# Performance work log

Measured on AMD Instinct MI355X. Metric: run time of the kernel, lower is better.

## Reference

```python
import jax, jax.numpy as jnp
import numpy as np

B, T, D = 2, 2048, 1024
H = 16
HD = D // H  # head_dim = 64 (kv_rank == embed_dim)
INT4_MIN, INT4_MAX = -8.0, 7.0


def _int4_quant_dequant(x):
    # per-token amax over last dim (head_dim), as in INT4Quantizer with 4-D input
    amax = jnp.max(jnp.abs(x), axis=-1, keepdims=True)
    amax = jnp.maximum(amax, 1e-5)
    scale = amax / 7.0
    q = jnp.clip(jnp.round(x / scale), INT4_MIN, INT4_MAX)  # stored as int8 in cache
    return q * scale


def setup_inputs() -> dict:
    key = jax.random.key(0)
    ks = jax.random.split(key, 11)
    s = 1.0 / np.sqrt(D)
    return {
        "query": jax.random.normal(ks[0], (B, T, D), jnp.float32),
        "key": jax.random.normal(ks[1], (B, T, D), jnp.float32),
        "value": jax.random.normal(ks[2], (B, T, D), jnp.float32),
        "Wq": jax.random.normal(ks[3], (D, D), jnp.float32) * s,
        "bq": jnp.zeros((D,), jnp.float32),
        "Wk": jax.random.normal(ks[4], (D, D), jnp.float32) * s,
        "bk": jnp.zeros((D,), jnp.float32),
        "Wv": jax.random.normal(ks[5], (D, D), jnp.float32) * s,
        "bv": jnp.zeros((D,), jnp.float32),
        "Wo": jax.random.normal(ks[6], (D, D), jnp.float32) * s,
        "bo": jnp.zeros((D,), jnp.float32),
    }


def reference(query, key, value, Wq, bq, Wk, bk, Wv, bv, Wo, bo):
    # projections (nn.Linear: x @ W.T + b)
    q = query @ Wq.T + bq
    k = key @ Wk.T + bk
    v = value @ Wv.T + bv
    # (B, T, D) -> (B, H, T, HD)
    q = q.reshape(B, T, H, HD).transpose(0, 2, 1, 3)
    k = k.reshape(B, T, H, HD).transpose(0, 2, 1, 3)
    v = v.reshape(B, T, H, HD).transpose(0, 2, 1, 3)
    # INT4 quantized KV cache update (use_cache=True): quantize -> scatter into
    # fresh cache -> dequantize the just-written block == quant/dequant of k, v
    k = _int4_quant_dequant(k)
    v = _int4_quant_dequant(v)
    # attention
    scale = HD ** (-0.5)
    attn = jnp.einsum("bhqd,bhkd->bhqk", q, k) * scale
    attn = jax.nn.softmax(attn.astype(jnp.float32), axis=-1).astype(query.dtype)
    out = jnp.einsum("bhqk,bhkd->bhqd", attn, v)
    out = out.transpose(0, 2, 1, 3).reshape(B, T, D)
    out = out @ Wo.T + bo
    return out
```

## Files before the change

### kernel.cpp

```cpp
#include <hip/hip_runtime.h>

typedef unsigned short u16;
typedef unsigned int u32;
typedef float f32x4 __attribute__((ext_vector_type(4)));
typedef float f32x16 __attribute__((ext_vector_type(16)));
typedef short s16x8 __attribute__((ext_vector_type(8)));
typedef u16 u16x8 __attribute__((ext_vector_type(8)));
typedef u16 u16x4 __attribute__((ext_vector_type(4)));
typedef u32 u32x4 __attribute__((ext_vector_type(4)));
typedef _Float16 h16x8 __attribute__((ext_vector_type(8)));
typedef _Float16 h16x2 __attribute__((ext_vector_type(2)));

#define B_ 2
#define T_ 2048
#define H_ 16
#define D_ 1024
#define HD_ 64
#define NTOK (B_*T_)

#define QSCALE 0.18033688011112042f

__device__ __forceinline__ u16 f2b(float f){
  u32 u = __float_as_uint(f);
  return (u16)((u + 0x7fffu + ((u>>16)&1u)) >> 16);
}
__device__ __forceinline__ float b2f(u16 h){ return __uint_as_float(((u32)h)<<16); }

__device__ __forceinline__ void gload_lds16(const u16* g, u16* s){
  __builtin_amdgcn_global_load_lds((const __attribute__((address_space(1))) void*)g,
                                   (__attribute__((address_space(3))) void*)s, 16, 0, 0);
}

template<int ROWS, int WAVES>
__device__ __forceinline__ void stage_tile(const u16* __restrict__ g, size_t ldg,
                                           u16* s, int tid){
  const int w = tid>>6, l = tid&63;
  const int rw = ROWS/WAVES;
  #pragma unroll
  for (int i=0;i<ROWS/(WAVES*8);i++){
    int r0 = w*rw + i*8;
    int r  = r0 + (l>>3);
    int u  = (l&7) ^ (r&7);
    gload_lds16(g + (size_t)r*ldg + (size_t)u*8, s + r0*64);
  }
}

__device__ __forceinline__ u16x8 read_frag(const u16* s, int r, int kk, int l){
  int u = (kk<<2) | (l>>4);
  int phys = u ^ (r&7);
  return *(const u16x8*)(s + r*64 + phys*8);
}
__device__ __forceinline__ u16x8 rfragT(const u16* s, int r, int ks, int hi){
  int phys = (ks*2 + hi) ^ (r&7);
  return *(const u16x8*)(s + r*64 + phys*8);
}

__device__ __forceinline__ void stage_tile32(const u16* __restrict__ g, size_t ldg,
                                             u16* s, int tid){
  const int w = tid>>6, l = tid&63;
  int r0 = w*16;
  int r  = r0 + (l>>2);
  int v  = (l&3) ^ ((r>>1)&3);
  gload_lds16(g + (size_t)r*ldg + (size_t)v*8, s + r0*32);
}
__device__ __forceinline__ u16x8 read_frag32(const u16* s, int r, int l){
  int phys = (l>>4) ^ ((r>>1)&3);
  return *(const u16x8*)(s + r*32 + phys*8);
}

__device__ __forceinline__ f32x4 mfma16_f16(u16x8 a, u16x8 b, f32x4 c){
  return __builtin_amdgcn_mfma_f32_16x16x32_f16(
      __builtin_bit_cast(h16x8,a), __builtin_bit_cast(h16x8,b), c, 0,0,0);
}
__device__ __forceinline__ f32x4 mfma16_bf16(u16x8 a, u16x8 b, f32x4 c){
  return __builtin_amdgcn_mfma_f32_16x16x32_bf16(
      __builtin_bit_cast(s16x8,a), __builtin_bit_cast(s16x8,b), c, 0,0,0);
}
__device__ __forceinline__ f32x16 mfma32_f16(u16x8 a, u16x8 b, f32x16 c){
  return __builtin_amdgcn_mfma_f32_32x32x16_f16(
      __builtin_bit_cast(h16x8,a), __builtin_bit_cast(h16x8,b), c, 0,0,0);
}

__device__ __forceinline__ float ex2(float x){
#if __has_builtin(__builtin_amdgcn_exp2f)
  return __builtin_amdgcn_exp2f(x);
#else
  return exp2f(x);
#endif
}
__device__ __forceinline__ u32 pk2(float a, float b){
  u16 x = __builtin_bit_cast(u16, (_Float16)a);
  u16 y = __builtin_bit_cast(u16, (_Float16)b);
  return (u32)x | ((u32)y<<16);
}
__device__ __forceinline__ float dot2acc(u32 wv, float c){
#if __has_builtin(__builtin_amdgcn_fdot2)
  h16x2 one2 = {(_Float16)1.0f, (_Float16)1.0f};
  return __builtin_amdgcn_fdot2(__builtin_bit_cast(h16x2, wv), one2, c, false);
#else
  h16x2 v = __builtin_bit_cast(h16x2, wv);
  return c + (float)v[0] + (float)v[1];
#endif
}

__device__ __forceinline__ void split_bf4(const float* in, u16* hi, u16* lo, int i){
  f32x4 v = ((const f32x4*)in)[i];
  u16x4 h, lw;
  #pragma unroll
  for (int j=0;j<4;j++){
    u16 hb = f2b(v[j]);
    h[j] = hb;
    lw[j] = f2b(v[j] - b2f(hb));
  }
  ((u16x4*)hi)[i] = h;
  ((u16x4*)lo)[i] = lw;
}
__device__ __forceinline__ void split_h4(const float* in, u16* out, int i){
  f32x4 v = ((const f32x4*)in)[i];
  u16x4 o;
  #pragma unroll
  for (int j=0;j<4;j++){
    _Float16 t = (_Float16)v[j];
    o[j] = __builtin_bit_cast(u16, t);
  }
  ((u16x4*)out)[i] = o;
}

__global__ void split_inputs_kernel(const float* __restrict__ q, const float* __restrict__ k,
                                    const float* __restrict__ v,
                                    u16* __restrict__ qh, u16* __restrict__ khi, u16* __restrict__ klo,
                                    u16* __restrict__ vhi, u16* __restrict__ vlo){
  int i = blockIdx.x*256 + threadIdx.x;
  int which = blockIdx.y;
  if (which==0)      split_h4 (q, qh, i);
  else if (which==1) split_bf4(k, khi, klo, i);
  else               split_bf4(v, vhi, vlo, i);
}

__global__ void split_weights_kernel(const float* __restrict__ wq, const float* __restrict__ wk,
                                     const float* __restrict__ wv, const float* __restrict__ wo,
                                     u16* __restrict__ wqh, u16* __restrict__ wkh, u16* __restrict__ wkl,
                                     u16* __restrict__ wvh, u16* __restrict__ wvl, u16* __restrict__ woh){
  int i = blockIdx.x*256 + threadIdx.x;
  int which = blockIdx.y;
  if (which==0)      split_h4 (wq, wqh, i);
  else if (which==1) split_bf4(wk, wkh, wkl, i);
  else if (which==2) split_bf4(wv, wvh, wvl, i);
  else               split_h4 (wo, woh, i);
}

template<int F16OUT>
__global__ __launch_bounds__(512)
void gemm1(const u16* __restrict__ Ah, const u16* __restrict__ Wh,
           const float* __restrict__ bias, void* __restrict__ Cout, float oscale)
{
  __shared__ u16 sA[2][128*64];
  __shared__ u16 sW[2][64*64];
  const int tid = threadIdx.x, l = tid&63, l15 = l&15, g = l>>4, w = tid>>6;
  const int wm = w>>1, wn = w&1;
  const int bm = blockIdx.x, bn = blockIdx.y;
  const u16* A0 = Ah + (size_t)bm*128*D_;
  const u16* W0 = Wh + (size_t)bn*64*D_;
  f32x4 acc[2][2] = {};

  stage_tile<128,8>(A0, D_, sA[0], tid);
  stage_tile<64 ,8>(W0, D_, sW[0], tid);
  __syncthreads();
  for (int t=0; t<D_/64; ++t){
    const int cur = t&1;
    if (t+1 < D_/64){
      stage_tile<128,8>(A0 + (t+1)*64, D_, sA[cur^1], tid);
      stage_tile<64 ,8>(W0 + (t+1)*64, D_, sW[cur^1], tid);
    }
    #pragma unroll
    for (int kk=0;kk<2;kk++){
      u16x8 af[2], wf[2];
      #pragma unroll
      for (int fm=0;fm<2;fm++) af[fm] = read_frag(sA[cur], wm*32+fm*16+l15, kk, l);
      #pragma unroll
      for (int fn=0;fn<2;fn++) wf[fn] = read_frag(sW[cur], wn*32+fn*16+l15, kk, l);
      #pragma unroll
      for (int fm=0;fm<2;fm++)
        #pragma unroll
        for (int fn=0;fn<2;fn++)
          acc[fm][fn] = mfma16_f16(af[fm], wf[fn], acc[fm][fn]);
    }
    __syncthreads();
  }

  #pragma unroll
  for (int fn=0; fn<2; fn++){
    int col = bn*64 + wn*32 + fn*16 + l15;
    float bv = bias[col];
    #pragma unroll
    for (int fm=0; fm<2; fm++){
      int r0 = bm*128 + wm*32 + fm*16 + g*4;
      #pragma unroll
      for (int j=0;j<4;j++){
        float v = (acc[fm][fn][j] + bv) * oscale;
        if constexpr (F16OUT){
          ((_Float16*)Cout)[(size_t)(r0+j)*D_ + col] = (_Float16)v;
        } else {
          ((float*)Cout)[(size_t)(r0+j)*D_ + col] = v;
        }
      }
    }
  }
}

template<int QMODE>
__global__ __launch_bounds__(512)
void gemm3_quant(const u16* __restrict__ Ah, const u16* __restrict__ Al,
                 const u16* __restrict__ Wh, const u16* __restrict__ Wl,
                 const float* __restrict__ bias, u16* __restrict__ Out)
{
  extern __shared__ u16 sm[];
  const int tid = threadIdx.x, l = tid&63, w = tid>>6, l15 = l&15, g = l>>4;
  const int wm = w>>1, wn = w&1;
  const int bm = blockIdx.x, bn = blockIdx.y;
  const u16* A0 = Ah + (size_t)bm*128*D_;
  const u16* A1 = Al + (size_t)bm*128*D_;
  const u16* W0 = Wh + (size_t)bn*128*D_;
  const u16* W1 = Wl + (size_t)bn*128*D_;
  constexpr int TS = 128*32;
  f32x4 acc[2][4] = {};

  auto stage = [&](int buf, int t){
    u16* base = sm + buf*4*TS;
    stage_tile32(A0 + t*32, D_, base       , tid);
    stage_tile32(A1 + t*32, D_, base +   TS, tid);
    stage_tile32(W0 + t*32, D_, base + 2*TS, tid);
    stage_tile32(W1 + t*32, D_, base + 3*TS, tid);
  };
  stage(0,0);
  __syncthreads();
  for (int t=0; t<D_/32; ++t){
    const int cur = t&1;
    if (t+1 < D_/32) stage(cur^1, t+1);
    const u16* base = sm + cur*4*TS;
    u16x8 ahh[2], ahl[2], whh[4], whl[4];
    #pragma unroll
    for (int fm=0;fm<2;fm++){
      ahh[fm] = read_frag32(base     , wm*32+fm*16+l15, l);
      ahl[fm] = read_frag32(base+  TS, wm*32+fm*16+l15, l);
    }
    #pragma unroll
    for (int fn=0;fn<4;fn++){
      whh[fn] = read_frag32(base+2*TS, wn*64+fn*16+l15, l);
      whl[fn] = read_frag32(base+3*TS, wn*64+fn*16+l15, l);
    }
    #pragma unroll
    for (int fm=0;fm<2;fm++)
      #pragma unroll
      for (int fn=0;fn<4;fn++){
        acc[fm][fn] = mfma16_bf16(ahh[fm], whh[fn], acc[fm][fn]);
        acc[fm][fn] = mfma16_bf16(ahh[fm], whl[fn], acc[fm][fn]);
        acc[fm][fn] = mfma16_bf16(ahl[fm], whh[fn], acc[fm][fn]);
      }
    __syncthreads();
  }

  #pragma unroll
  for (int fn=0;fn<4;fn++){
    float bv = bias[bn*128 + wn*64 + fn*16 + l15];
    #pragma unroll
    for (int fm=0;fm<2;fm++)
      #pragma unroll
      for (int j=0;j<4;j++) acc[fm][fn][j] += bv;
  }

  u16 (*sdq)[136] = (u16(*)[136])sm;
  #pragma unroll
  for (int fm=0;fm<2;fm++)
    #pragma unroll
    for (int j=0;j<4;j++){
      float a = 0.f;
      #pragma unroll
      for (int fn=0;fn<4;fn++) a = fmaxf(a, fabsf(acc[fm][fn][j]));
      a = fmaxf(a, __shfl_xor(a,1)); a = fmaxf(a, __shfl_xor(a,2));
      a = fmaxf(a, __shfl_xor(a,4)); a = fmaxf(a, __shfl_xor(a,8));
      a = fmaxf(a, 1e-5f);
      float scale = a / 7.0f;
      int row = wm*32 + fm*16 + g*4 + j;
      #pragma unroll
      for (int fn=0;fn<4;fn++){
        float q = rintf(acc[fm][fn][j] / scale);
        q = fminf(fmaxf(q, -8.f), 7.f);
        _Float16 dq = (_Float16)(q * scale);
        int col = wn*64 + fn*16 + l15;
        if (QMODE==1) sdq[row][col] = __builtin_bit_cast(u16, dq);
        else          sdq[col][row] = __builtin_bit_cast(u16, dq);
      }
    }
  __syncthreads();

  if (QMODE==1){
    int r = tid>>2, seg = tid&3;
    u16* dst = Out + (size_t)(bm*128 + r)*D_ + bn*128 + seg*32;
    #pragma unroll
    for (int i=0;i<4;i++)
      *(u16x8*)(dst + i*8) = *(const u16x8*)&sdq[r][seg*32 + i*8];
  } else {
    int cc = tid>>2, seg = tid&3;
    int hh = 2*bn + (cc>>6), dd = cc&63, b = bm>>4;
    u16* dst = Out + ((size_t)((b*H_+hh)*HD_ + dd))*T_ + (bm&15)*128 + seg*32;
    #pragma unroll
    for (int i=0;i<4;i++)
      *(u16x8*)(dst + i*8) = *(const u16x8*)&sdq[cc][seg*32 + i*8];
  }
}

__global__ __launch_bounds__(256)
void attn_kernel(const _Float16* __restrict__ Qp, const u16* __restrict__ Kdq,
                 const u16* __restrict__ Vt, _Float16* __restrict__ Aout)
{
  __shared__ u16 sK[2][64*64];
  __shared__ u16 sV[2][64*64];
  __shared__ float sRl[128];
  const int tid = threadIdx.x, l = tid&63, c = l&31, hi = l>>5, w = tid>>6;
  const int d = blockIdx.x;
  const int xcd = d & 7, slot = d >> 3;
  const int bh = xcd*4 + (slot>>4);
  const int qb = slot & 15;
  const int b = bh>>4, h = bh&15;

  u16x8 qf[4];
  {
    const u16* qrow = (const u16*)Qp + (size_t)(b*T_ + qb*128 + w*32 + c)*D_ + h*HD_;
    #pragma unroll
    for (int ks=0;ks<4;ks++)
      qf[ks] = *(const u16x8*)(qrow + ks*16 + hi*8);
  }

  f32x16 o0 = {}, o1 = {};
  float lsp = 0.f;

  const u16* Kb = Kdq + (size_t)(b*T_)*D_ + h*HD_;
  const u16* Vb = Vt  + (size_t)((b*H_+h)*HD_)*T_;

  stage_tile<64,4>(Kb, D_, sK[0], tid);
  stage_tile<64,4>(Vb, T_, sV[0], tid);
  __syncthreads();

  for (int kt=0; kt<T_/64; kt++){
    const int cur = kt&1;
    if (kt+1 < T_/64){
      stage_tile<64,4>(Kb + (size_t)((kt+1)*64)*D_, D_, sK[cur^1], tid);
      stage_tile<64,4>(Vb + (kt+1)*64,              T_, sV[cur^1], tid);
    }

    u16x8 vf0[4], vf1[4];
    #pragma unroll
    for (int ks=0;ks<4;ks++){
      vf0[ks] = rfragT(sV[cur],      c, ks, hi);
      vf1[ks] = rfragT(sV[cur], 32 + c, ks, hi);
    }

    #pragma unroll
    for (int kb=0;kb<2;kb++){
      f32x16 s = {};
      #pragma unroll
      for (int ks=0;ks<4;ks++){
        u16x8 kf = rfragT(sK[cur], kb*32 + c, ks, hi);
        s = mfma32_f16(kf, qf[ks], s);
      }
      float p[16];
      #pragma unroll
      for (int r=0;r<16;r++) p[r] = ex2(s[r]);
      u32 x0 = pk2(p[0],p[1]),   x1 = pk2(p[2],p[3]);
      u32 x2 = pk2(p[4],p[5]),   x3 = pk2(p[6],p[7]);
      u32 x4 = pk2(p[8],p[9]),   x5 = pk2(p[10],p[11]);
      u32 x6 = pk2(p[12],p[13]), x7 = pk2(p[14],p[15]);
      lsp = dot2acc(x0,lsp); lsp = dot2acc(x1,lsp);
      lsp = dot2acc(x2,lsp); lsp = dot2acc(x3,lsp);
      lsp = dot2acc(x4,lsp); lsp = dot2acc(x5,lsp);
      lsp = dot2acc(x6,lsp); lsp = dot2acc(x7,lsp);
      u32 y0 = __shfl_xor(x0,32), y1 = __shfl_xor(x1,32);
      u32 y2 = __shfl_xor(x2,32), y3 = __shfl_xor(x3,32);
      u32 y4 = __shfl_xor(x4,32), y5 = __shfl_xor(x5,32);
      u32 y6 = __shfl_xor(x6,32), y7 = __shfl_xor(x7,32);
      const bool hb = (hi != 0);
      u32x4 pw0 = { hb ? y2 : x0, hb ? y3 : x1, hb ? x2 : y0, hb ? x3 : y1 };
      u32x4 pw1 = { hb ? y6 : x4, hb ? y7 : x5, hb ? x6 : y4, hb ? x7 : y5 };
      u16x8 pa0 = __builtin_bit_cast(u16x8, pw0);
      u16x8 pa1 = __builtin_bit_cast(u16x8, pw1);
      o0 = mfma32_f16(pa0, vf0[kb*2+0], o0);
      o1 = mfma32_f16(pa0, vf1[kb*2+0], o1);
      o0 = mfma32_f16(pa1, vf0[kb*2+1], o0);
      o1 = mfma32_f16(pa1, vf1[kb*2+1], o1);
    }
    __syncthreads();
  }

  float lt = lsp + __shfl_xor(lsp, 32);
  if (l < 32) sRl[w*32 + c] = 1.0f / lt;
  __syncthreads();

  #pragma unroll
  for (int r=0;r<16;r++){
    int crow = (r&3) + 8*(r>>2) + 4*hi;
    float rl = sRl[w*32 + crow];
    int qr = qb*128 + w*32 + crow;
    _Float16* arow = Aout + (size_t)(b*T_+qr)*D_ + h*HD_;
    arow[c]      = (_Float16)(o0[r]*rl);
    arow[32 + c] = (_Float16)(o1[r]*rl);
  }
}

extern "C" void kernel_launch(void* const* d_in, const int* in_sizes, int n_in,
                              void* d_out, int out_size, void* d_ws, size_t ws_size,
                              hipStream_t stream)
{
  (void)in_sizes; (void)n_in; (void)out_size; (void)ws_size;
  const float* query = (const float*)d_in[0];
  const float* key   = (const float*)d_in[1];
  const float* value = (const float*)d_in[2];
  const float* Wq = (const float*)d_in[3];
  const float* bq = (const float*)d_in[4];
  const float* Wk = (const float*)d_in[5];
  const float* bk = (const float*)d_in[6];
  const float* Wv = (const float*)d_in[7];
  const float* bv = (const float*)d_in[8];
  const float* Wo = (const float*)d_in[9];
  const float* bo = (const float*)d_in[10];
  float* out = (float*)d_out;

  char* p = (char*)d_ws;
  auto take = [&](size_t n){ char* r = p; p += (n + 255) & ~(size_t)255; return r; };
  const size_t big = (size_t)NTOK*D_*2;
  const size_t wsz = (size_t)D_*D_*2;

  u16* q_h  = (u16*)take(big);
  u16* khi  = (u16*)take(big);  u16* klo = (u16*)take(big);
  u16* vhi  = (u16*)take(big);  u16* vlo = (u16*)take(big);
  u16* wq_h = (u16*)take(wsz);
  u16* wkh  = (u16*)take(wsz);  u16* wkl = (u16*)take(wsz);
  u16* wvh  = (u16*)take(wsz);  u16* wvl = (u16*)take(wsz);
  u16* wo_h = (u16*)take(wsz);
  u16*  Qp  = (u16*)take(big);
  u16*  Kdq = (u16*)take(big);
  u16*  Vtp = (u16*)take(big);
  u16*  Ao  = (u16*)take(big);

  split_inputs_kernel <<<dim3(NTOK*D_/4/256, 3), 256, 0, stream>>>(
      query, key, value, q_h, khi, klo, vhi, vlo);
  split_weights_kernel<<<dim3(D_*D_/4/256, 4), 256, 0, stream>>>(
      Wq, Wk, Wv, Wo, wq_h, wkh, wkl, wvh, wvl, wo_h);

  gemm1<1><<<dim3(32,16), 512, 0, stream>>>(q_h, wq_h, bq, Qp, QSCALE);
  gemm3_quant<1><<<dim3(32,8), 512, 64*1024, stream>>>(khi, klo, wkh, wkl, bk, Kdq);
  gemm3_quant<2><<<dim3(32,8), 512, 64*1024, stream>>>(vhi, vlo, wvh, wvl, bv, Vtp);

  attn_kernel<<<512, 256, 0, stream>>>((const _Float16*)Qp, Kdq, Vtp, (_Float16*)Ao);

  gemm1<0><<<dim3(32,16), 512, 0, stream>>>(Ao, wo_h, bo, out, 1.0f);
}
```

Measured before the change: 182.3 us.

## Split attention KV range across two blocks and combine partials in a separate kernel

The attention grid doubles to 1024 blocks, and each block processes half of the key sequence. Blocks write unnormalized fp32 partial outputs and row sums into reused workspace buffers, and a new combine kernel sums the two halves and normalizes. The change also replaces the fdot2 row-sum and cross-lane shuffles with plain fp32 adds and cvt_pkrtz packing, loads V fragments per kb with a different layout, and adds an occupancy hint. This raises parallelism and occupancy, at the cost of an extra launch and fp32 partial-result traffic. The register layout of P changes, and correctness depends on the new V fragment indexing matching it.

```diff
diff --git a/kernel.cpp b/kernel.cpp
--- a/kernel.cpp
+++ b/kernel.cpp
@@ -93,13 +93,12 @@
   u16 y = __builtin_bit_cast(u16, (_Float16)b);
   return (u32)x | ((u32)y<<16);
 }
-__device__ __forceinline__ float dot2acc(u32 wv, float c){
-#if __has_builtin(__builtin_amdgcn_fdot2)
-  h16x2 one2 = {(_Float16)1.0f, (_Float16)1.0f};
-  return __builtin_amdgcn_fdot2(__builtin_bit_cast(h16x2, wv), one2, c, false);
+__device__ __forceinline__ u32 pkrtz(float a, float b){
+#if __has_builtin(__builtin_amdgcn_cvt_pkrtz)
+  auto r = __builtin_amdgcn_cvt_pkrtz(a, b);
+  return __builtin_bit_cast(u32, r);
 #else
-  h16x2 v = __builtin_bit_cast(h16x2, wv);
-  return c + (float)v[0] + (float)v[1];
+  return pk2(a, b);
 #endif
 }
 
@@ -310,19 +309,21 @@
   }
 }
 
-__global__ __launch_bounds__(256)
+__global__ __launch_bounds__(256, 4)
 void attn_kernel(const _Float16* __restrict__ Qp, const u16* __restrict__ Kdq,
-                 const u16* __restrict__ Vt, _Float16* __restrict__ Aout)
+                 const u16* __restrict__ Vt, float* __restrict__ po,
+                 float* __restrict__ pl)
 {
   __shared__ u16 sK[2][64*64];
   __shared__ u16 sV[2][64*64];
-  __shared__ float sRl[128];
   const int tid = threadIdx.x, l = tid&63, c = l&31, hi = l>>5, w = tid>>6;
-  const int d = blockIdx.x;
-  const int xcd = d & 7, slot = d >> 3;
-  const int bh = xcd*4 + (slot>>4);
-  const int qb = slot & 15;
+  const int dsp = blockIdx.x;
+  const int xcd = dsp & 7, slot = dsp >> 3;
+  const int bh = xcd*4 + (slot>>5);
+  const int rem = slot & 31;
+  const int qb = rem >> 1, sp = rem & 1;
   const int b = bh>>4, h = bh&15;
+  const int off = 4*hi;
 
   u16x8 qf[4];
   {
@@ -335,76 +336,100 @@
   f32x16 o0 = {}, o1 = {};
   float lsp = 0.f;
 
-  const u16* Kb = Kdq + (size_t)(b*T_)*D_ + h*HD_;
-  const u16* Vb = Vt  + (size_t)((b*H_+h)*HD_)*T_;
+  const u16* Kb = Kdq + (size_t)(b*T_ + sp*1024)*D_ + h*HD_;
+  const u16* Vb = Vt  + (size_t)(bh*HD_)*T_ + sp*1024;
 
   stage_tile<64,4>(Kb, D_, sK[0], tid);
   stage_tile<64,4>(Vb, T_, sV[0], tid);
   __syncthreads();
 
-  for (int kt=0; kt<T_/64; kt++){
+  for (int kt=0; kt<16; kt++){
     const int cur = kt&1;
-    if (kt+1 < T_/64){
+    if (kt+1 < 16){
       stage_tile<64,4>(Kb + (size_t)((kt+1)*64)*D_, D_, sK[cur^1], tid);
       stage_tile<64,4>(Vb + (kt+1)*64,              T_, sV[cur^1], tid);
     }
-
-    u16x8 vf0[4], vf1[4];
-    #pragma unroll
-    for (int ks=0;ks<4;ks++){
-      vf0[ks] = rfragT(sV[cur],      c, ks, hi);
-      vf1[ks] = rfragT(sV[cur], 32 + c, ks, hi);
-    }
+    const u16* sKc = sK[cur];
+    const u16* sVc = sV[cur];
 
     #pragma unroll
     for (int kb=0;kb<2;kb++){
       f32x16 s = {};
       #pragma unroll
       for (int ks=0;ks<4;ks++){
-        u16x8 kf = rfragT(sK[cur], kb*32 + c, ks, hi);
+        u16x8 kf = rfragT(sKc, kb*32 + c, ks, hi);
         s = mfma32_f16(kf, qf[ks], s);
       }
+      u16x8 vfr[2][2];
+      #pragma unroll
+      for (int vr=0;vr<2;vr++){
+        int rv = vr*32 + c;
+        int rx = rv & 7;
+        const u16* vb = sVc + rv*64 + off;
+        #pragma unroll
+        for (int part=0;part<2;part++){
+          int u0 = 4*kb + 2*part;
+          u16x4 lo4 = *(const u16x4*)(vb + ((u0  ) ^ rx)*8);
+          u16x4 hi4 = *(const u16x4*)(vb + ((u0+1) ^ rx)*8);
+          struct { u16x4 a, b; } t{lo4, hi4};
+          vfr[vr][part] = __builtin_bit_cast(u16x8, t);
+        }
+      }
       float p[16];
       #pragma unroll
       for (int r=0;r<16;r++) p[r] = ex2(s[r]);
-      u32 x0 = pk2(p[0],p[1]),   x1 = pk2(p[2],p[3]);
-      u32 x2 = pk2(p[4],p[5]),   x3 = pk2(p[6],p[7]);
-      u32 x4 = pk2(p[8],p[9]),   x5 = pk2(p[10],p[11]);
-      u32 x6 = pk2(p[12],p[13]), x7 = pk2(p[14],p[15]);
-      lsp = dot2acc(x0,lsp); lsp = dot2acc(x1,lsp);
-      lsp = dot2acc(x2,lsp); lsp = dot2acc(x3,lsp);
-      lsp = dot2acc(x4,lsp); lsp = dot2acc(x5,lsp);
-      lsp = dot2acc(x6,lsp); lsp = dot2acc(x7,lsp);
-      u32 y0 = __shfl_xor(x0,32), y1 = __shfl_xor(x1,32);
-      u32 y2 = __shfl_xor(x2,32), y3 = __shfl_xor(x3,32);
-      u32 y4 = __shfl_xor(x4,32), y5 = __shfl_xor(x5,32);
-      u32 y6 = __shfl_xor(x6,32), y7 = __shfl_xor(x7,32);
-      const bool hb = (hi != 0);
-      u32x4 pw0 = { hb ? y2 : x0, hb ? y3 : x1, hb ? x2 : y0, hb ? x3 : y1 };
-      u32x4 pw1 = { hb ? y6 : x4, hb ? y7 : x5, hb ? x6 : y4, hb ? x7 : y5 };
+      {
+        float t0 = (p[0]+p[1]) + (p[2]+p[3]);
+        float t1 = (p[4]+p[5]) + (p[6]+p[7]);
+        float t2 = (p[8]+p[9]) + (p[10]+p[11]);
+        float t3 = (p[12]+p[13]) + (p[14]+p[15]);
+        lsp += (t0+t1) + (t2+t3);
+      }
+      u32x4 pw0 = { pkrtz(p[0],p[1]),  pkrtz(p[2],p[3]),
+                    pkrtz(p[4],p[5]),  pkrtz(p[6],p[7]) };
+      u32x4 pw1 = { pkrtz(p[8],p[9]),  pkrtz(p[10],p[11]),
+                    pkrtz(p[12],p[13]),pkrtz(p[14],p[15]) };
       u16x8 pa0 = __builtin_bit_cast(u16x8, pw0);
       u16x8 pa1 = __builtin_bit_cast(u16x8, pw1);
-      o0 = mfma32_f16(pa0, vf0[kb*2+0], o0);
-      o1 = mfma32_f16(pa0, vf1[kb*2+0], o1);
-      o0 = mfma32_f16(pa1, vf0[kb*2+1], o0);
-      o1 = mfma32_f16(pa1, vf1[kb*2+1], o1);
+      o0 = mfma32_f16(pa0, vfr[0][0], o0);
+      o0 = mfma32_f16(pa1, vfr[0][1], o0);
+      o1 = mfma32_f16(pa0, vfr[1][0], o1);
+      o1 = mfma32_f16(pa1, vfr[1][1], o1);
     }
     __syncthreads();
   }
 
   float lt = lsp + __shfl_xor(lsp, 32);
-  if (l < 32) sRl[w*32 + c] = 1.0f / lt;
-  __syncthreads();
-
+  if (hi == 0) pl[(size_t)(sp*32 + bh)*T_ + qb*128 + w*32 + c] = lt;
+
+  float* pob = po + ((size_t)(sp*32 + bh)*T_ + qb*128 + w*32)*HD_;
   #pragma unroll
   for (int r=0;r<16;r++){
     int crow = (r&3) + 8*(r>>2) + 4*hi;
-    float rl = sRl[w*32 + crow];
-    int qr = qb*128 + w*32 + crow;
-    _Float16* arow = Aout + (size_t)(b*T_+qr)*D_ + h*HD_;
-    arow[c]      = (_Float16)(o0[r]*rl);
-    arow[32 + c] = (_Float16)(o1[r]*rl);
-  }
+    pob[crow*HD_ + c]      = o0[r];
+    pob[crow*HD_ + 32 + c] = o1[r];
+  }
+}
+
+__global__ __launch_bounds__(256)
+void combine_kernel(const float* __restrict__ po, const float* __restrict__ pl,
+                    u16* __restrict__ Ao)
+{
+  int i = blockIdx.x*256 + threadIdx.x;
+  int d4 = (i & 15) * 4;
+  int t  = (i >> 4) & (T_-1);
+  int bh = i >> 15;
+  size_t r0 = ((size_t)bh*T_ + t);
+  f32x4 a = *(const f32x4*)(po + r0*HD_ + d4);
+  f32x4 b = *(const f32x4*)(po + (r0 + (size_t)32*T_)*HD_ + d4);
+  float lt = pl[r0] + pl[r0 + (size_t)32*T_];
+  float rl = 1.0f / lt;
+  u16x4 o;
+  #pragma unroll
+  for (int j=0;j<4;j++)
+    o[j] = __builtin_bit_cast(u16, (_Float16)((a[j]+b[j])*rl));
+  int bb = bh>>4, hh = bh&15;
+  *(u16x4*)(Ao + ((size_t)(bb*T_ + t))*D_ + hh*HD_ + d4) = o;
 }
 
 extern "C" void kernel_launch(void* const* d_in, const int* in_sizes, int n_in,
@@ -442,6 +467,9 @@
   u16*  Vtp = (u16*)take(big);
   u16*  Ao  = (u16*)take(big);
 
+  float* po = (float*)khi;
+  float* pl = (float*)wq_h;
+
   split_inputs_kernel <<<dim3(NTOK*D_/4/256, 3), 256, 0, stream>>>(
       query, key, value, q_h, khi, klo, vhi, vlo);
   split_weights_kernel<<<dim3(D_*D_/4/256, 4), 256, 0, stream>>>(
@@ -451,7 +479,8 @@
   gemm3_quant<1><<<dim3(32,8), 512, 64*1024, stream>>>(khi, klo, wkh, wkl, bk, Kdq);
   gemm3_quant<2><<<dim3(32,8), 512, 64*1024, stream>>>(vhi, vlo, wvh, wvl, bv, Vtp);
 
-  attn_kernel<<<512, 256, 0, stream>>>((const _Float16*)Qp, Kdq, Vtp, (_Float16*)Ao);
+  attn_kernel<<<1024, 256, 0, stream>>>((const _Float16*)Qp, Kdq, Vtp, po, pl);
+  combine_kernel<<<4096, 256, 0, stream>>>(po, pl, Ao);
 
   gemm1<0><<<dim3(32,16), 512, 0, stream>>>(Ao, wo_h, bo, out, 1.0f);
 }
```

New measurement: 184.4 us. Within noise of the previous version (+1.1%).
